# Optimization experiments

Measured on AMD Instinct MI355X. Metric: run time of the kernel, lower is better.

## Reference

```python
import jax, jax.numpy as jnp
import numpy as np

K = 7           # kernel_size
GROUPS = 16     # channels // group_channels = 256 // 16
GC = 16         # group_channels
BN_EPS = 1e-5


def setup_inputs() -> dict:
    key = jax.random.key(0)
    ks = jax.random.split(key, 6)
    B, C, H, W = 4, 256, 64, 64
    cr = C // 4                      # reduction_ratio = 4
    k2g = K * K * GROUPS             # conv2 out channels = 784
    return {
        "feature_map": jax.random.normal(ks[0], (B, C, H, W), jnp.float32),
        "guide_map":   jax.random.normal(ks[1], (B, C, H, W), jnp.float32),
        "w1": jax.random.normal(ks[2], (cr, C), jnp.float32) * 0.05,
        "bn_gamma": jnp.ones((cr,), jnp.float32),
        "bn_beta":  jnp.zeros((cr,), jnp.float32),
        "bn_mean":  jax.random.normal(ks[3], (cr,), jnp.float32) * 0.1,
        "bn_var":   jax.random.uniform(ks[4], (cr,), jnp.float32, 0.5, 1.5),
        "w2": jax.random.normal(ks[5], (k2g, cr), jnp.float32) * 0.05,
        "b2": jnp.zeros((k2g,), jnp.float32),
    }


def reference(feature_map, guide_map, w1, bn_gamma, bn_beta, bn_mean, bn_var, w2, b2):
    b, c, h, w = feature_map.shape
    # conv1 (1x1) + BN (inference stats) + ReLU
    x = jnp.einsum("oc,bchw->bohw", w1, guide_map)
    inv = bn_gamma / jnp.sqrt(bn_var + BN_EPS)
    x = x * inv[None, :, None, None] + (bn_beta - bn_mean * inv)[None, :, None, None]
    x = jax.nn.relu(x)
    # conv2 (1x1): dynamic per-pixel kernel weights -> [b, groups, k^2, h, w]
    weight = jnp.einsum("oc,bchw->bohw", w2, x) + b2[None, :, None, None]
    weight = weight.reshape(b, GROUPS, K * K, h, w)
    # unfold feature_map (same padding, stride 1) -> [b, c, k^2, h, w]
    pad = (K - 1) // 2
    fp = jnp.pad(feature_map, ((0, 0), (0, 0), (pad, pad), (pad, pad)))
    patches = jnp.stack(
        [fp[:, :, i:i + h, j:j + w] for i in range(K) for j in range(K)], axis=2
    )
    patches = patches.reshape(b, GROUPS, GC, K * K, h, w)
    # dynamic weighted aggregation over kernel positions, then residual
    out = jnp.einsum("bgkhw,bgckhw->bgchw", weight, patches)
    return out.reshape(b, c, h, w) + feature_map
```

## Files before the change

kernel.cpp:

```cpp
#include <hip/hip_runtime.h>

#define BN_EPS 1e-5f

typedef __bf16 bf16_t;
typedef __bf16 bf16x8 __attribute__((ext_vector_type(8)));
typedef __bf16 bf16x4 __attribute__((ext_vector_type(4)));
typedef __bf16 bf16x2 __attribute__((ext_vector_type(2)));
typedef float  floatx4 __attribute__((ext_vector_type(4)));

#define MFMA16(a, b, c) __builtin_amdgcn_mfma_f32_16x16x32_bf16((a), (b), (c), 0, 0, 0)

#define XT_OFF 0

#define GTP 264

__global__ __launch_bounds__(512) void conv1_k(
    const float* __restrict__ guide, const float* __restrict__ w1,
    const float* __restrict__ gamma, const float* __restrict__ beta,
    const float* __restrict__ mean,  const float* __restrict__ var,
    bf16_t* __restrict__ xT)
{
    __shared__ __attribute__((aligned(16))) bf16_t gTs[64 * GTP];
    const int b = blockIdx.x >> 6, h = blockIdx.x & 63;
    const int t = threadIdx.x;

    const float* gsrc = guide + (size_t)b * 256 * 4096 + h * 64;
#pragma unroll
    for (int i = 0; i < 16; ++i) {
        const int idx = i * 512 + t;
        const int c2 = idx >> 6, p = idx & 63;
        const float g0 = gsrc[(size_t)(2 * c2) * 4096 + p];
        const float g1 = gsrc[(size_t)(2 * c2 + 1) * 4096 + p];
        bf16x2 pk; pk[0] = (bf16_t)g0; pk[1] = (bf16_t)g1;
        *(bf16x2*)&gTs[p * GTP + 2 * c2] = pk;
    }
    __syncthreads();

    const int wv = t >> 6, ln = t & 63, l15 = ln & 15, q = ln >> 4;
    const int ot = wv & 3;
    const int ph = wv >> 2;
    const int o = ot * 16 + l15;
    const float iv = gamma[o] * rsqrtf(var[o] + BN_EPS);

    floatx4 acc[2] = {};
#pragma unroll
    for (int ks = 0; ks < 8; ++ks) {
        const float* wp = w1 + o * 256 + ks * 32 + q * 8;
        const float4 a0 = *(const float4*)(wp);
        const float4 a1 = *(const float4*)(wp + 4);
        bf16x8 a;
        a[0] = (bf16_t)(a0.x * iv); a[1] = (bf16_t)(a0.y * iv);
        a[2] = (bf16_t)(a0.z * iv); a[3] = (bf16_t)(a0.w * iv);
        a[4] = (bf16_t)(a1.x * iv); a[5] = (bf16_t)(a1.y * iv);
        a[6] = (bf16_t)(a1.z * iv); a[7] = (bf16_t)(a1.w * iv);
#pragma unroll
        for (int nt = 0; nt < 2; ++nt) {
            const bf16x8 bb = *(const bf16x8*)&gTs[(ph * 32 + nt * 16 + l15) * GTP + ks * 32 + q * 8];
            acc[nt] = MFMA16(a, bb, acc[nt]);
        }
    }
    float bi[4];
#pragma unroll
    for (int j = 0; j < 4; ++j) {
        const int o2 = ot * 16 + q * 4 + j;
        const float iv2 = gamma[o2] * rsqrtf(var[o2] + BN_EPS);
        bi[j] = beta[o2] - mean[o2] * iv2;
    }
#pragma unroll
    for (int nt = 0; nt < 2; ++nt) {
        const int p = ph * 32 + nt * 16 + l15;
        bf16x4 v;
#pragma unroll
        for (int j = 0; j < 4; ++j) v[j] = (bf16_t)fmaxf(acc[nt][j] + bi[j], 0.f);
        *(bf16x4*)(xT + ((size_t)(b * 64 + h) * 64 + p) * 64 + ot * 16 + q * 4) = v;
    }
}

#define FSR 72
#define FSC 576
#define WGP 136

__global__ __launch_bounds__(256) void fused_k(
    const bf16_t* __restrict__ xT, const float* __restrict__ w2,
    const float* __restrict__ b2,  const float* __restrict__ feat,
    float* __restrict__ out)
{
    __shared__ __attribute__((aligned(16))) float  fs[16 * FSC];
    __shared__ __attribute__((aligned(16))) bf16_t wgs[49 * WGP];

    const int g = blockIdx.x & 15;
    const int rest = blockIdx.x >> 4;
    const int b = rest >> 5, hp = rest & 31;
    const int h0 = hp * 2;
    const int t = threadIdx.x;
    const int wv = t >> 6, ln = t & 63, l15 = ln & 15, q = ln >> 4;

#pragma unroll
    for (int i = 0; i < 9; ++i) {
        const int u = i * 256 + t;
        const int c = u / 144, rem = u - c * 144;
        const int rr = rem / 18, qq = rem - rr * 18;
        const int hh = h0 - 3 + rr;
        float4 v = {0.f, 0.f, 0.f, 0.f};
        if (qq >= 1 && qq <= 16 && hh >= 0 && hh < 64)
            v = *(const float4*)(feat + ((size_t)(b * 256 + g * 16 + c) * 64 + hh) * 64 + (qq - 1) * 4);
        *(float4*)&fs[c * FSC + rr * FSR + qq * 4] = v;
    }

    {
        floatx4 acc[4][2] = {};
        const bf16_t* brow = xT + ((size_t)(b * 64 + h0) * 64 + wv * 32) * 64;
#pragma unroll
        for (int ks = 0; ks < 2; ++ks) {
            bf16x8 bfr[2];
            bfr[0] = *(const bf16x8*)(brow + l15 * 64 + ks * 32 + q * 8);
            bfr[1] = *(const bf16x8*)(brow + (16 + l15) * 64 + ks * 32 + q * 8);
#pragma unroll
            for (int mt = 0; mt < 4; ++mt) {
                int row = mt * 16 + l15; if (row > 48) row = 48;
                const float* wp = w2 + (size_t)(g * 49 + row) * 64 + ks * 32 + q * 8;
                const float4 a0 = *(const float4*)(wp);
                const float4 a1 = *(const float4*)(wp + 4);
                bf16x8 a;
                a[0] = (bf16_t)a0.x; a[1] = (bf16_t)a0.y; a[2] = (bf16_t)a0.z; a[3] = (bf16_t)a0.w;
                a[4] = (bf16_t)a1.x; a[5] = (bf16_t)a1.y; a[6] = (bf16_t)a1.z; a[7] = (bf16_t)a1.w;
                acc[mt][0] = MFMA16(a, bfr[0], acc[mt][0]);
                acc[mt][1] = MFMA16(a, bfr[1], acc[mt][1]);
            }
        }
#pragma unroll
        for (int mt = 0; mt < 4; ++mt) {
#pragma unroll
            for (int j = 0; j < 4; ++j) {
                const int k = mt * 16 + q * 4 + j;
                if (k < 49) {
                    const float bias = b2[g * 49 + k];
                    wgs[k * WGP + wv * 32 + l15]      = (bf16_t)(acc[mt][0][j] + bias);
                    wgs[k * WGP + wv * 32 + 16 + l15] = (bf16_t)(acc[mt][1][j] + bias);
                }
            }
        }
    }
    __syncthreads();

    const int wq = t & 15, r = (t >> 4) & 1, cp = t >> 5;
    const int w0 = wq * 4;
    const int ch0 = cp * 2;

    float acc[2][4] = {};
#pragma unroll
    for (int di = 0; di < 7; ++di) {
        const int ri = r + di;
        float f0[12], f1[12];
        {
            const float* p0 = &fs[ch0 * FSC + ri * FSR + w0];
            const float* p1 = p0 + FSC;
#pragma unroll
            for (int qj = 0; qj < 3; ++qj) {
                const floatx4 a = *(const floatx4*)(p0 + qj * 4);
                const floatx4 bq = *(const floatx4*)(p1 + qj * 4);
#pragma unroll
                for (int j = 0; j < 4; ++j) { f0[qj * 4 + j] = a[j]; f1[qj * 4 + j] = bq[j]; }
            }
        }
        const bf16_t* wrow = &wgs[(di * 7) * WGP + r * 64 + w0];
#pragma unroll
        for (int dj = 0; dj < 7; ++dj) {
            const bf16x4 wb = *(const bf16x4*)(wrow + dj * WGP);
#pragma unroll
            for (int x = 0; x < 4; ++x) {
                const float wf = (float)wb[x];
                acc[0][x] = fmaf(wf, f0[x + dj + 1], acc[0][x]);
                acc[1][x] = fmaf(wf, f1[x + dj + 1], acc[1][x]);
            }
        }
    }

#pragma unroll
    for (int c = 0; c < 2; ++c) {
        const floatx4 res = *(const floatx4*)&fs[(ch0 + c) * FSC + (r + 3) * FSR + 4 + w0];
        const size_t ob = ((size_t)(b * 256 + g * 16 + ch0 + c) * 64 + h0 + r) * 64 + w0;
        float4 o;
        o.x = acc[c][0] + res[0]; o.y = acc[c][1] + res[1];
        o.z = acc[c][2] + res[2]; o.w = acc[c][3] + res[3];
        *(float4*)(out + ob) = o;
    }
}

extern "C" void kernel_launch(void* const* d_in, const int* in_sizes, int n_in,
                              void* d_out, int out_size, void* d_ws, size_t ws_size,
                              hipStream_t stream) {
    const float* feature = (const float*)d_in[0];
    const float* guide   = (const float*)d_in[1];
    const float* w1      = (const float*)d_in[2];
    const float* gamma   = (const float*)d_in[3];
    const float* beta    = (const float*)d_in[4];
    const float* mean    = (const float*)d_in[5];
    const float* var     = (const float*)d_in[6];
    const float* w2      = (const float*)d_in[7];
    const float* b2      = (const float*)d_in[8];
    float* out = (float*)d_out;

    bf16_t* xT = (bf16_t*)((char*)d_ws + XT_OFF);

    conv1_k<<<256, 512, 0, stream>>>(guide, w1, gamma, beta, mean, var, xT);
    fused_k<<<2048, 256, 0, stream>>>(xT, w2, b2, feature, out);
}
```

Baseline: 123.6 us.

## Split fused conv2+aggregation into separate kernels via global bf16 weight buffer

The fused kernel is split in two. conv2_k computes the per-pixel dynamic weights and writes them to a global bf16 workspace. A new agg_k kernel loads a 4-row feature tile per group into shared memory and reads the weights directly from global memory. The intent is to shrink per-block shared memory and raise occupancy in the aggregation stage, and to cut halo overhead by using taller row tiles. In exchange it adds a third launch and a roughly 12.8 MB global write and read round trip, with strided uncoalesced-ish weight loads.

```diff
diff --git a/kernel.cpp b/kernel.cpp
--- a/kernel.cpp
+++ b/kernel.cpp
@@ -11,6 +11,7 @@
 #define MFMA16(a, b, c) __builtin_amdgcn_mfma_f32_16x16x32_bf16((a), (b), (c), 0, 0, 0)
 
 #define XT_OFF 0
+#define WG_OFF (4u << 20)
 
 #define GTP 264
 
@@ -76,16 +77,12 @@
     }
 }
 
-#define FSR 72
-#define FSC 576
 #define WGP 136
 
-__global__ __launch_bounds__(256) void fused_k(
+__global__ __launch_bounds__(256) void conv2_k(
     const bf16_t* __restrict__ xT, const float* __restrict__ w2,
-    const float* __restrict__ b2,  const float* __restrict__ feat,
-    float* __restrict__ out)
+    const float* __restrict__ b2,  bf16_t* __restrict__ wgG)
 {
-    __shared__ __attribute__((aligned(16))) float  fs[16 * FSC];
     __shared__ __attribute__((aligned(16))) bf16_t wgs[49 * WGP];
 
     const int g = blockIdx.x & 15;
@@ -94,18 +91,6 @@
     const int h0 = hp * 2;
     const int t = threadIdx.x;
     const int wv = t >> 6, ln = t & 63, l15 = ln & 15, q = ln >> 4;
-
-#pragma unroll
-    for (int i = 0; i < 9; ++i) {
-        const int u = i * 256 + t;
-        const int c = u / 144, rem = u - c * 144;
-        const int rr = rem / 18, qq = rem - rr * 18;
-        const int hh = h0 - 3 + rr;
-        float4 v = {0.f, 0.f, 0.f, 0.f};
-        if (qq >= 1 && qq <= 16 && hh >= 0 && hh < 64)
-            v = *(const float4*)(feat + ((size_t)(b * 256 + g * 16 + c) * 64 + hh) * 64 + (qq - 1) * 4);
-        *(float4*)&fs[c * FSC + rr * FSR + qq * 4] = v;
-    }
 
     {
         floatx4 acc[4][2] = {};
@@ -143,11 +128,55 @@
     }
     __syncthreads();
 
-    const int wq = t & 15, r = (t >> 4) & 1, cp = t >> 5;
+    const size_t obase = (size_t)(g * 49) * 16384 + (size_t)(b * 64 + h0) * 64;
+#pragma unroll
+    for (int i = 0; i < 7; ++i) {
+        const int u = i * 256 + t;
+        if (u < 1568) {
+            const int k = u >> 5, j = u & 31;
+            *(bf16x4*)(wgG + obase + (size_t)k * 16384 + j * 4) =
+                *(const bf16x4*)&wgs[k * WGP + j * 4];
+        }
+    }
+}
+
+#define FSR 72
+#define FSC 720
+
+__global__ __launch_bounds__(512, 6) void agg_k(
+    const bf16_t* __restrict__ wgG, const float* __restrict__ feat,
+    float* __restrict__ out)
+{
+    __shared__ __attribute__((aligned(16))) float fs[16 * FSC];
+
+    const int g = blockIdx.x & 15;
+    const int rest = blockIdx.x >> 4;
+    const int b = rest >> 4, hq = rest & 15;
+    const int h0 = hq * 4;
+    const int t = threadIdx.x;
+
+#pragma unroll
+    for (int i = 0; i < 6; ++i) {
+        const int u = i * 512 + t;
+        if (u < 2880) {
+            const int c = u / 180, rem = u - c * 180;
+            const int rr = rem / 18, qq = rem - rr * 18;
+            const int hh = h0 - 3 + rr;
+            float4 v = {0.f, 0.f, 0.f, 0.f};
+            if (qq >= 1 && qq <= 16 && hh >= 0 && hh < 64)
+                v = *(const float4*)(feat + ((size_t)(b * 256 + g * 16 + c) * 64 + hh) * 64 + (qq - 1) * 4);
+            *(float4*)&fs[c * FSC + rr * FSR + qq * 4] = v;
+        }
+    }
+    __syncthreads();
+
+    const int wq = t & 15, r = (t >> 4) & 3, cp = t >> 6;
     const int w0 = wq * 4;
     const int ch0 = cp * 2;
 
     float acc[2][4] = {};
+    const bf16_t* wbase = wgG + (size_t)(g * 49) * 16384
+                              + (size_t)(b * 64 + h0 + r) * 64 + w0;
 #pragma unroll
     for (int di = 0; di < 7; ++di) {
         const int ri = r + di;
@@ -163,10 +192,10 @@
                 for (int j = 0; j < 4; ++j) { f0[qj * 4 + j] = a[j]; f1[qj * 4 + j] = bq[j]; }
             }
         }
-        const bf16_t* wrow = &wgs[(di * 7) * WGP + r * 64 + w0];
+        const bf16_t* wrow = wbase + (size_t)(di * 7) * 16384;
 #pragma unroll
         for (int dj = 0; dj < 7; ++dj) {
-            const bf16x4 wb = *(const bf16x4*)(wrow + dj * WGP);
+            const bf16x4 wb = *(const bf16x4*)(wrow + (size_t)dj * 16384);
 #pragma unroll
             for (int x = 0; x < 4; ++x) {
                 const float wf = (float)wb[x];
@@ -201,8 +230,10 @@
     const float* b2      = (const float*)d_in[8];
     float* out = (float*)d_out;
 
-    bf16_t* xT = (bf16_t*)((char*)d_ws + XT_OFF);
+    bf16_t* xT  = (bf16_t*)((char*)d_ws + XT_OFF);
+    bf16_t* wgG = (bf16_t*)((char*)d_ws + WG_OFF);
 
     conv1_k<<<256, 512, 0, stream>>>(guide, w1, gamma, beta, mean, var, xT);
-    fused_k<<<2048, 256, 0, stream>>>(xT, w2, b2, feature, out);
-}
+    conv2_k<<<2048, 256, 0, stream>>>(xT, w2, b2, wgG);
+    agg_k<<<1024, 512, 0, stream>>>(wgG, feature, out);
+}
```

After: 137.1 us. 11.0% more time.

## Process one output row per block in fused kernel instead of two

Applied to the files above, without the earlier changes.

Each fused-kernel block now handles a single image row per group instead of a pair of rows, doubling the grid to 4096 blocks. The feature halo tile shrinks from 8 to 7 rows and the weight LDS tile halves, each wave computing one 16-row tile of conv2 output across 64 pixels. It also reduces per-thread work to one channel. The intent is more parallelism and smaller LDS footprint for higher occupancy. The cost is less halo reuse: feature rows are reloaded more often (7 rows per output row versus 4), and w2 is loaded by twice as many blocks.

```diff
diff --git a/kernel.cpp b/kernel.cpp
--- a/kernel.cpp
+++ b/kernel.cpp
@@ -77,8 +77,8 @@
 }
 
 #define FSR 72
-#define FSC 576
-#define WGP 136
+#define FSC 504
+#define WGP 72
 
 __global__ __launch_bounds__(256) void fused_k(
     const bf16_t* __restrict__ xT, const float* __restrict__ w2,
@@ -90,99 +90,87 @@
 
     const int g = blockIdx.x & 15;
     const int rest = blockIdx.x >> 4;
-    const int b = rest >> 5, hp = rest & 31;
-    const int h0 = hp * 2;
+    const int b = rest >> 6, h = rest & 63;
     const int t = threadIdx.x;
     const int wv = t >> 6, ln = t & 63, l15 = ln & 15, q = ln >> 4;
 
 #pragma unroll
-    for (int i = 0; i < 9; ++i) {
+    for (int i = 0; i < 8; ++i) {
         const int u = i * 256 + t;
-        const int c = u / 144, rem = u - c * 144;
-        const int rr = rem / 18, qq = rem - rr * 18;
-        const int hh = h0 - 3 + rr;
-        float4 v = {0.f, 0.f, 0.f, 0.f};
-        if (qq >= 1 && qq <= 16 && hh >= 0 && hh < 64)
-            v = *(const float4*)(feat + ((size_t)(b * 256 + g * 16 + c) * 64 + hh) * 64 + (qq - 1) * 4);
-        *(float4*)&fs[c * FSC + rr * FSR + qq * 4] = v;
+        if (u < 2016) {
+            const int c = u / 126, rem = u - c * 126;
+            const int rr = rem / 18, qq = rem - rr * 18;
+            const int hh = h - 3 + rr;
+            float4 v = {0.f, 0.f, 0.f, 0.f};
+            if (qq >= 1 && qq <= 16 && hh >= 0 && hh < 64)
+                v = *(const float4*)(feat + ((size_t)(b * 256 + g * 16 + c) * 64 + hh) * 64 + (qq - 1) * 4);
+            *(float4*)&fs[c * FSC + rr * FSR + qq * 4] = v;
+        }
     }
 
     {
-        floatx4 acc[4][2] = {};
-        const bf16_t* brow = xT + ((size_t)(b * 64 + h0) * 64 + wv * 32) * 64;
+        floatx4 acc[4] = {};
+        const bf16_t* brow = xT + ((size_t)(b * 64 + h) * 64) * 64;
+        int row = wv * 16 + l15; if (row > 48) row = 48;
 #pragma unroll
         for (int ks = 0; ks < 2; ++ks) {
-            bf16x8 bfr[2];
-            bfr[0] = *(const bf16x8*)(brow + l15 * 64 + ks * 32 + q * 8);
-            bfr[1] = *(const bf16x8*)(brow + (16 + l15) * 64 + ks * 32 + q * 8);
+            const float* wp = w2 + (size_t)(g * 49 + row) * 64 + ks * 32 + q * 8;
+            const float4 a0 = *(const float4*)(wp);
+            const float4 a1 = *(const float4*)(wp + 4);
+            bf16x8 a;
+            a[0] = (bf16_t)a0.x; a[1] = (bf16_t)a0.y; a[2] = (bf16_t)a0.z; a[3] = (bf16_t)a0.w;
+            a[4] = (bf16_t)a1.x; a[5] = (bf16_t)a1.y; a[6] = (bf16_t)a1.z; a[7] = (bf16_t)a1.w;
 #pragma unroll
-            for (int mt = 0; mt < 4; ++mt) {
-                int row = mt * 16 + l15; if (row > 48) row = 48;
-                const float* wp = w2 + (size_t)(g * 49 + row) * 64 + ks * 32 + q * 8;
-                const float4 a0 = *(const float4*)(wp);
-                const float4 a1 = *(const float4*)(wp + 4);
-                bf16x8 a;
-                a[0] = (bf16_t)a0.x; a[1] = (bf16_t)a0.y; a[2] = (bf16_t)a0.z; a[3] = (bf16_t)a0.w;
-                a[4] = (bf16_t)a1.x; a[5] = (bf16_t)a1.y; a[6] = (bf16_t)a1.z; a[7] = (bf16_t)a1.w;
-                acc[mt][0] = MFMA16(a, bfr[0], acc[mt][0]);
-                acc[mt][1] = MFMA16(a, bfr[1], acc[mt][1]);
+            for (int nt = 0; nt < 4; ++nt) {
+                const bf16x8 bb = *(const bf16x8*)(brow + (nt * 16 + l15) * 64 + ks * 32 + q * 8);
+                acc[nt] = MFMA16(a, bb, acc[nt]);
             }
         }
 #pragma unroll
-        for (int mt = 0; mt < 4; ++mt) {
+        for (int j = 0; j < 4; ++j) {
+            const int k = wv * 16 + q * 4 + j;
+            if (k < 49) {
+                const float bias = b2[g * 49 + k];
 #pragma unroll
-            for (int j = 0; j < 4; ++j) {
-                const int k = mt * 16 + q * 4 + j;
-                if (k < 49) {
-                    const float bias = b2[g * 49 + k];
-                    wgs[k * WGP + wv * 32 + l15]      = (bf16_t)(acc[mt][0][j] + bias);
-                    wgs[k * WGP + wv * 32 + 16 + l15] = (bf16_t)(acc[mt][1][j] + bias);
-                }
+                for (int nt = 0; nt < 4; ++nt)
+                    wgs[k * WGP + nt * 16 + l15] = (bf16_t)(acc[nt][j] + bias);
             }
         }
     }
     __syncthreads();
 
-    const int wq = t & 15, r = (t >> 4) & 1, cp = t >> 5;
+    const int wq = t & 15, cp = t >> 4;
     const int w0 = wq * 4;
-    const int ch0 = cp * 2;
 
-    float acc[2][4] = {};
+    float acc4[4] = {};
 #pragma unroll
     for (int di = 0; di < 7; ++di) {
-        const int ri = r + di;
-        float f0[12], f1[12];
+        float f0[12];
         {
-            const float* p0 = &fs[ch0 * FSC + ri * FSR + w0];
-            const float* p1 = p0 + FSC;
+            const float* p0 = &fs[cp * FSC + di * FSR + w0];
 #pragma unroll
             for (int qj = 0; qj < 3; ++qj) {
                 const floatx4 a = *(const floatx4*)(p0 + qj * 4);
-                const floatx4 bq = *(const floatx4*)(p1 + qj * 4);
 #pragma unroll
-                for (int j = 0; j < 4; ++j) { f0[qj * 4 + j] = a[j]; f1[qj * 4 + j] = bq[j]; }
+                for (int j = 0; j < 4; ++j) f0[qj * 4 + j] = a[j];
             }
         }
-        const bf16_t* wrow = &wgs[(di * 7) * WGP + r * 64 + w0];
+        const bf16_t* wrow = &wgs[(di * 7) * WGP + w0];
 #pragma unroll
         for (int dj = 0; dj < 7; ++dj) {
             const bf16x4 wb = *(const bf16x4*)(wrow + dj * WGP);
 #pragma unroll
-            for (int x = 0; x < 4; ++x) {
-                const float wf = (float)wb[x];
-                acc[0][x] = fmaf(wf, f0[x + dj + 1], acc[0][x]);
-                acc[1][x] = fmaf(wf, f1[x + dj + 1], acc[1][x]);
-            }
+            for (int x = 0; x < 4; ++x)
+                acc4[x] = fmaf((float)wb[x], f0[x + dj + 1], acc4[x]);
         }
     }
 
-#pragma unroll
-    for (int c = 0; c < 2; ++c) {
-        const floatx4 res = *(const floatx4*)&fs[(ch0 + c) * FSC + (r + 3) * FSR + 4 + w0];
-        const size_t ob = ((size_t)(b * 256 + g * 16 + ch0 + c) * 64 + h0 + r) * 64 + w0;
+    {
+        const floatx4 res = *(const floatx4*)&fs[cp * FSC + 3 * FSR + 4 + w0];
+        const size_t ob = ((size_t)(b * 256 + g * 16 + cp) * 64 + h) * 64 + w0;
         float4 o;
-        o.x = acc[c][0] + res[0]; o.y = acc[c][1] + res[1];
-        o.z = acc[c][2] + res[2]; o.w = acc[c][3] + res[3];
+        o.x = acc4[0] + res[0]; o.y = acc4[1] + res[1];
+        o.z = acc4[2] + res[2]; o.w = acc4[3] + res[3];
         *(float4*)(out + ob) = o;
     }
 }
@@ -204,5 +192,5 @@
     bf16_t* xT = (bf16_t*)((char*)d_ws + XT_OFF);
 
     conv1_k<<<256, 512, 0, stream>>>(guide, w1, gamma, beta, mean, var, xT);
-    fused_k<<<2048, 256, 0, stream>>>(xT, w2, b2, feature, out);
+    fused_k<<<4096, 256, 0, stream>>>(xT, w2, b2, feature, out);
 }
```

Measured after the change: 135.6 us. +9.7%, slower.

## Defer feature LDS stores, pad channel stride, double-buffer aggregation loads

Applied to the files above, without the earlier changes.

The feature tile loads are kept in registers until after the conv2 MFMA phase, so global-load latency overlaps with the weight-generation work instead of stalling before it. The channel stride in shared memory is padded from 576 to 584 floats to reduce LDS bank conflicts between the two channels each thread reads. The 7x7 aggregation loop is restructured into an explicit two-stage register double buffer so LDS loads for the next row are issued ahead of the FMAs for the current row. This raises register pressure (36 floats held across the MFMA phase plus doubled staging buffers), which may lower occupancy and slightly enlarges the shared-memory footprint.

```diff
diff --git a/kernel.cpp b/kernel.cpp
--- a/kernel.cpp
+++ b/kernel.cpp
@@ -77,7 +77,7 @@
 }
 
 #define FSR 72
-#define FSC 576
+#define FSC 584
 #define WGP 136
 
 __global__ __launch_bounds__(256) void fused_k(
@@ -95,6 +95,8 @@
     const int t = threadIdx.x;
     const int wv = t >> 6, ln = t & 63, l15 = ln & 15, q = ln >> 4;
 
+    float4 fsv[9];
+    int    fsa[9];
 #pragma unroll
     for (int i = 0; i < 9; ++i) {
         const int u = i * 256 + t;
@@ -104,7 +106,8 @@
         float4 v = {0.f, 0.f, 0.f, 0.f};
         if (qq >= 1 && qq <= 16 && hh >= 0 && hh < 64)
             v = *(const float4*)(feat + ((size_t)(b * 256 + g * 16 + c) * 64 + hh) * 64 + (qq - 1) * 4);
-        *(float4*)&fs[c * FSC + rr * FSR + qq * 4] = v;
+        fsv[i] = v;
+        fsa[i] = c * FSC + rr * FSR + qq * 4;
     }
 
     {
@@ -141,40 +144,64 @@
             }
         }
     }
+
+#pragma unroll
+    for (int i = 0; i < 9; ++i)
+        *(float4*)&fs[fsa[i]] = fsv[i];
     __syncthreads();
 
     const int wq = t & 15, r = (t >> 4) & 1, cp = t >> 5;
     const int w0 = wq * 4;
     const int ch0 = cp * 2;
 
+#define LOAD_STAGE(di, WA, FA, FB) do {                                        \
+        const bf16_t* wrow_ = &wgs[((di) * 7) * WGP + r * 64 + w0];            \
+        _Pragma("unroll")                                                      \
+        for (int dj = 0; dj < 7; ++dj) WA[dj] = *(const bf16x4*)(wrow_ + dj * WGP); \
+        const float* p0_ = &fs[ch0 * FSC + ((di) + r) * FSR + w0];             \
+        const float* p1_ = p0_ + FSC;                                          \
+        _Pragma("unroll")                                                      \
+        for (int qj = 0; qj < 3; ++qj) {                                       \
+            FA[qj] = *(const floatx4*)(p0_ + qj * 4);                          \
+            FB[qj] = *(const floatx4*)(p1_ + qj * 4);                          \
+        }                                                                      \
+    } while (0)
+
+#define FMA_STAGE(WA, FA, FB) do {                                             \
+        _Pragma("unroll")                                                      \
+        for (int dj = 0; dj < 7; ++dj) {                                       \
+            const bf16x4 wb_ = WA[dj];                                         \
+            _Pragma("unroll")                                                  \
+            for (int x = 0; x < 4; ++x) {                                      \
+                const int e = x + dj + 1;                                      \
+                const float wf_ = (float)wb_[x];                               \
+                acc[0][x] = fmaf(wf_, FA[e >> 2][e & 3], acc[0][x]);           \
+                acc[1][x] = fmaf(wf_, FB[e >> 2][e & 3], acc[1][x]);           \
+            }                                                                  \
+        }                                                                      \
+    } while (0)
+
     float acc[2][4] = {};
-#pragma unroll
-    for (int di = 0; di < 7; ++di) {
-        const int ri = r + di;
-        float f0[12], f1[12];
-        {
-            const float* p0 = &fs[ch0 * FSC + ri * FSR + w0];
-            const float* p1 = p0 + FSC;
-#pragma unroll
-            for (int qj = 0; qj < 3; ++qj) {
-                const floatx4 a = *(const floatx4*)(p0 + qj * 4);
-                const floatx4 bq = *(const floatx4*)(p1 + qj * 4);
-#pragma unroll
-                for (int j = 0; j < 4; ++j) { f0[qj * 4 + j] = a[j]; f1[qj * 4 + j] = bq[j]; }
-            }
-        }
-        const bf16_t* wrow = &wgs[(di * 7) * WGP + r * 64 + w0];
-#pragma unroll
-        for (int dj = 0; dj < 7; ++dj) {
-            const bf16x4 wb = *(const bf16x4*)(wrow + dj * WGP);
-#pragma unroll
-            for (int x = 0; x < 4; ++x) {
-                const float wf = (float)wb[x];
-                acc[0][x] = fmaf(wf, f0[x + dj + 1], acc[0][x]);
-                acc[1][x] = fmaf(wf, f1[x + dj + 1], acc[1][x]);
-            }
-        }
-    }
+    bf16x4 waA[7], waB[7];
+    floatx4 faA[3], fbA[3], faB[3], fbB[3];
+
+    LOAD_STAGE(0, waA, faA, fbA);
+    LOAD_STAGE(1, waB, faB, fbB);
+    FMA_STAGE(waA, faA, fbA);
+    LOAD_STAGE(2, waA, faA, fbA);
+    FMA_STAGE(waB, faB, fbB);
+    LOAD_STAGE(3, waB, faB, fbB);
+    FMA_STAGE(waA, faA, fbA);
+    LOAD_STAGE(4, waA, faA, fbA);
+    FMA_STAGE(waB, faB, fbB);
+    LOAD_STAGE(5, waB, faB, fbB);
+    FMA_STAGE(waA, faA, fbA);
+    LOAD_STAGE(6, waA, faA, fbA);
+    FMA_STAGE(waB, faB, fbB);
+    FMA_STAGE(waA, faA, fbA);
+
+#undef LOAD_STAGE
+#undef FMA_STAGE
 
 #pragma unroll
     for (int c = 0; c < 2; ++c) {
```

Result: slower. 129.0 us (+4.4%).
